# Optimization experiments

Hardware: AMD Instinct MI355X
Metric: run time of the kernel (lower is better)

## Reference

```python
import jax, jax.numpy as jnp
import numpy as np

N_CLASSES = 4
ALPHA = 2.0
BIG = jnp.float32(1e9)  # stands in for +inf at non-site pixels


def _dt1d_sq(f):
    # Exact 1D squared distance transform along the last axis:
    # out[i] = min_j f[j] + (i - j)^2  (brute-force lower envelope, fully vectorized)
    n = f.shape[-1]
    i = jnp.arange(n, dtype=f.dtype)
    d2 = (i[:, None] - i[None, :]) ** 2  # [n, n]
    return jnp.min(f[..., None, :] + d2, axis=-1)


def _edt_sq(sites):
    # Exact squared Euclidean distance to the nearest True pixel (separable 2D DT).
    f = jnp.where(sites, jnp.float32(0.0), BIG)
    f = _dt1d_sq(f)                                  # pass along W
    f = jnp.swapaxes(_dt1d_sq(jnp.swapaxes(f, -1, -2)), -1, -2)  # pass along H
    return f


def _distance_field(img):
    # Mirrors HausdorffDTLoss.distance_field:
    #   fg_dist = edt(fg_mask)  (distance to nearest bg pixel, 0 on bg)
    #   bg_dist = edt(~fg_mask) (distance to nearest fg pixel, 0 on fg)
    #   field = fg_dist + bg_dist if fg_mask.any() else 0
    fg = img > 0.5                                   # [B, H, W] bool
    fg_dist = jnp.sqrt(_edt_sq(~fg))                 # dist to nearest background
    bg_dist = jnp.sqrt(_edt_sq(fg))                  # dist to nearest foreground
    any_fg = jnp.any(fg, axis=(-2, -1), keepdims=True)
    return jnp.where(any_fg, fg_dist + bg_dist, jnp.float32(0.0))


def reference(pred, target):
    # pred: [B, 4, H, W] logits; target: [B, H, W] int labels in [0, 4)
    probs = jax.nn.softmax(pred, axis=1)
    tgt = jnp.moveaxis(jax.nn.one_hot(target, N_CLASSES, dtype=probs.dtype), -1, 1)  # [B,4,H,W]
    total = jnp.float32(0.0)
    for i in range(N_CLASSES):
        p = probs[:, i]
        t = tgt[:, i]
        pred_dt = jax.lax.stop_gradient(_distance_field(p))
        target_dt = jax.lax.stop_gradient(_distance_field(t))
        pred_error = (p - t) ** 2
        distance = pred_dt ** ALPHA + target_dt ** ALPHA
        total = total + jnp.mean(pred_error * distance)
    return total / N_CLASSES


def setup_inputs() -> dict:
    key = jax.random.key(0)
    k1, k2 = jax.random.split(key)
    pred = jax.random.normal(k1, (4, 4, 256, 256), dtype=jnp.float32)
    target = jax.random.randint(k2, (4, 256, 256), 0, 4).astype(jnp.int32)
    return {"pred": pred, "target": target}
```

## Files before the change

### kernel.cpp

```cpp
#include <hip/hip_runtime.h>

#define HH 256
#define WW 256
#define NB 4
#define NC 4
#define NPIX (HH*WW)
#define NIMG (NB*NC)
#define TOTAL (NB*NC*HH*WW)
#define INF_G (1<<30)

__device__ __forceinline__ float wave_reduce(float v) {
    #pragma unroll
    for (int off = 32; off > 0; off >>= 1) v += __shfl_down(v, off);
    return v;
}

__device__ __forceinline__ int nearest_dist(const unsigned long long* m, int x) {
    int best = 0x7fffffff;
    #pragma unroll
    for (int w = 0; w < 4; ++w) {
        unsigned long long mm = m[w];
        if (!mm) continue;
        int rel = x - (w << 6);
        unsigned long long lmask = (rel >= 63) ? ~0ull
                                 : ((rel < 0) ? 0ull : ((2ull << (rel & 63)) - 1ull));
        unsigned long long lm = mm & lmask;
        if (lm) best = min(best, rel - (63 - __clzll(lm)));
        unsigned long long rmask = (rel <= 0) ? ~0ull
                                 : ((rel > 63) ? 0ull : (~0ull << (rel & 63)));
        unsigned long long rm = mm & rmask;
        if (rm) best = min(best, (__ffsll((long long)rm) - 1) - rel);
    }
    return best;
}

__global__ void fused_rows(const float* __restrict__ pred, const int* __restrict__ target,
                           uint2* __restrict__ buf) {
    int blk = blockIdx.x;
    int b = blk >> 8, y = blk & 255;
    int x = threadIdx.x;

    const float* base = pred + (((size_t)b * NC) * HH + y) * WW + x;
    float v0 = base[0 * (size_t)NPIX];
    float v1 = base[1 * (size_t)NPIX];
    float v2 = base[2 * (size_t)NPIX];
    float v3 = base[3 * (size_t)NPIX];
    float m = fmaxf(fmaxf(v0, v1), fmaxf(v2, v3));
    float e0 = expf(v0 - m), e1 = expf(v1 - m), e2 = expf(v2 - m), e3 = expf(v3 - m);
    float inv = 1.0f / (e0 + e1 + e2 + e3);
    float p[4] = { e0 * inv, e1 * inv, e2 * inv, e3 * inv };

    int tc = target[((size_t)b * HH + y) * WW + x];

    __shared__ unsigned long long mP[4][4], mT[4][4];
    int lane = x & 63, wave = x >> 6;
    #pragma unroll
    for (int c = 0; c < 4; ++c) {
        unsigned long long bp = __ballot(p[c] > 0.5f);
        unsigned long long bt = __ballot(tc == c);
        if (lane == 0) { mP[c][wave] = bp; mT[c][wave] = bt; }
    }
    __syncthreads();

    #pragma unroll
    for (int c = 0; c < 4; ++c) {
        bool fgP = p[c] > 0.5f;
        bool fgT = (tc == c);
        unsigned long long flipP = fgP ? ~0ull : 0ull;
        unsigned long long flipT = fgT ? ~0ull : 0ull;
        unsigned long long selP[4], selT[4];
        #pragma unroll
        for (int w = 0; w < 4; ++w) {
            selP[w] = mP[c][w] ^ flipP;
            selT[w] = mT[c][w] ^ flipT;
        }
        int dP = nearest_dist(selP, x);
        int dT = nearest_dist(selT, x);

        unsigned int codeP = (fgP ? 0x100u : 0u) | ((dP > 255) ? 0x200u : (unsigned int)dP);
        unsigned int codeT = (fgT ? 0x100u : 0u) | ((dT > 255) ? 0x200u : (unsigned int)dT);

        float t = fgT ? 1.0f : 0.0f;
        float d = p[c] - t;
        float pe = d * d;

        size_t ti = (((size_t)(b * NC + c)) * WW + x) * HH + y;
        uint2 outv;
        outv.x = codeP | (codeT << 16);
        outv.y = __float_as_uint(pe);
        buf[ti] = outv;
    }
}

__global__ void dt_cols_loss(const uint2* __restrict__ buf, float* __restrict__ partials) {
    int blk = blockIdx.x;
    int img = blk >> 8, x = blk & 255;
    int y = threadIdx.x;
    int lane = y & 63, wv = y >> 6;

    size_t ti = (((size_t)img) * WW + x) * HH + y;

    __shared__ int g[4][HH];
    __shared__ int sF[8];
    __shared__ float sred[4];

    uint2 v = buf[ti];
    unsigned int cP = v.x & 0xFFFFu, cT = v.x >> 16;
    int fgP = (cP >> 8) & 1, emP = (cP >> 9) & 1, dP = (int)(cP & 0xFFu);
    int fgT = (cT >> 8) & 1, emT = (cT >> 9) & 1, dT = (int)(cT & 0xFFu);
    int vP = emP ? INF_G : dP * dP;
    int vT = emT ? INF_G : dT * dT;
    g[0][y] = fgP ? vP : 0;
    g[1][y] = fgP ? 0 : vP;
    g[2][y] = fgT ? vT : 0;
    g[3][y] = fgT ? 0 : vT;

    unsigned long long bP = __ballot(fgP || !emP);
    unsigned long long bT = __ballot(fgT || !emT);
    if (lane == 0) { sF[wv] = (bP != 0ull); sF[4 + wv] = (bT != 0ull); }
    __syncthreads();

    int hs1 = sF[0] | sF[1] | sF[2] | sF[3];
    int hs3 = sF[4] | sF[5] | sF[6] | sF[7];

    const int* gP = fgP ? g[0] : g[1];
    const int* gT = fgT ? g[2] : g[3];

    float dtP, dtT;
    {
        int best = gP[y];
        for (int s = 1; s < HH; ++s) {
            int ss = s * s;
            if (ss >= best) break;
            int jm = y - s;
            if (jm >= 0) best = min(best, gP[jm] + ss);
            int jp = y + s;
            if (jp < HH) best = min(best, gP[jp] + ss);
        }
        dtP = (best >= INF_G) ? sqrtf(1.0e9f) : sqrtf((float)best);
    }
    {
        int best = gT[y];
        for (int s = 1; s < HH; ++s) {
            int ss = s * s;
            if (ss >= best) break;
            int jm = y - s;
            if (jm >= 0) best = min(best, gT[jm] + ss);
            int jp = y + s;
            if (jp < HH) best = min(best, gT[jp] + ss);
        }
        dtT = (best >= INF_G) ? sqrtf(1.0e9f) : sqrtf((float)best);
    }

    float pe = __uint_as_float(v.y);
    float pd = hs1 ? dtP : 0.0f;
    float td = hs3 ? dtT : 0.0f;
    float val = pe * (pd * pd + td * td);

    val = wave_reduce(val);
    if (lane == 0) sred[wv] = val;
    __syncthreads();
    if (y == 0)
        partials[blk] = sred[0] + sred[1] + sred[2] + sred[3];
}

__global__ void final_kernel(const float* __restrict__ partials, float* __restrict__ out) {
    float a = 0.0f;
    for (int i = threadIdx.x; i < 4096; i += 256) a += partials[i];
    a = wave_reduce(a);
    __shared__ float s[4];
    int lane = threadIdx.x & 63, wave = threadIdx.x >> 6;
    if (lane == 0) s[wave] = a;
    __syncthreads();
    if (threadIdx.x == 0)
        out[0] = (s[0] + s[1] + s[2] + s[3]) * (1.0f / (float)TOTAL);
}

extern "C" void kernel_launch(void* const* d_in, const int* in_sizes, int n_in,
                              void* d_out, int out_size, void* d_ws, size_t ws_size,
                              hipStream_t stream) {
    const float* pred  = (const float*)d_in[0];
    const int* target  = (const int*)d_in[1];
    float* out = (float*)d_out;

    float* ws = (float*)d_ws;
    uint2* buf      = (uint2*)ws;
    float* partials = ws + 2097152;

    fused_rows<<<NB * HH, 256, 0, stream>>>(pred, target, buf);
    dt_cols_loss<<<NIMG * WW, 256, 0, stream>>>(buf, partials);
    final_kernel<<<1, 256, 0, stream>>>(partials, out);
}
```

Baseline: 34.41 us.

## Pass compact row bitmasks between kernels and fold final reduction into atomics

The first kernel now writes only per-row ballot bitmasks and a transposed squared-error array, instead of per-pixel packed distance codes. The row-wise nearest-distance search moves into the column kernel, which loads the image's bitmasks into shared memory and handles four columns per 1024-thread block. The separate final reduction kernel is removed: each block atomically adds its scaled partial sum into the output, which the first kernel zeroes. This cuts intermediate global traffic and one launch, at the cost of repeating the row search in the column kernel and a non-deterministic float atomic summation order.

```diff
diff --git a/kernel.cpp b/kernel.cpp
--- a/kernel.cpp
+++ b/kernel.cpp
@@ -34,11 +34,14 @@
     return best;
 }
 
-__global__ void fused_rows(const float* __restrict__ pred, const int* __restrict__ target,
-                           uint2* __restrict__ buf) {
+__global__ void build_masks(const float* __restrict__ pred, const int* __restrict__ target,
+                            unsigned long long* __restrict__ masks, float* __restrict__ peT,
+                            float* __restrict__ out) {
     int blk = blockIdx.x;
     int b = blk >> 8, y = blk & 255;
     int x = threadIdx.x;
+
+    if (blk == 0 && x == 0) out[0] = 0.0f;
 
     const float* base = pred + (((size_t)b * NC) * HH + y) * WW + x;
     float v0 = base[0 * (size_t)NPIX];
@@ -52,79 +55,82 @@
 
     int tc = target[((size_t)b * HH + y) * WW + x];
 
-    __shared__ unsigned long long mP[4][4], mT[4][4];
-    int lane = x & 63, wave = x >> 6;
+    __shared__ unsigned long long sm[NC][2][4];
+    int lane = x & 63, wv = x >> 6;
     #pragma unroll
     for (int c = 0; c < 4; ++c) {
         unsigned long long bp = __ballot(p[c] > 0.5f);
         unsigned long long bt = __ballot(tc == c);
-        if (lane == 0) { mP[c][wave] = bp; mT[c][wave] = bt; }
+        if (lane == 0) { sm[c][0][wv] = bp; sm[c][1][wv] = bt; }
+        float t = (tc == c) ? 1.0f : 0.0f;
+        float d = p[c] - t;
+        peT[(((size_t)(b * NC + c)) * WW + x) * HH + y] = d * d;
     }
     __syncthreads();
 
-    #pragma unroll
-    for (int c = 0; c < 4; ++c) {
-        bool fgP = p[c] > 0.5f;
-        bool fgT = (tc == c);
-        unsigned long long flipP = fgP ? ~0ull : 0ull;
-        unsigned long long flipT = fgT ? ~0ull : 0ull;
-        unsigned long long selP[4], selT[4];
-        #pragma unroll
-        for (int w = 0; w < 4; ++w) {
-            selP[w] = mP[c][w] ^ flipP;
-            selT[w] = mT[c][w] ^ flipT;
-        }
-        int dP = nearest_dist(selP, x);
-        int dT = nearest_dist(selT, x);
-
-        unsigned int codeP = (fgP ? 0x100u : 0u) | ((dP > 255) ? 0x200u : (unsigned int)dP);
-        unsigned int codeT = (fgT ? 0x100u : 0u) | ((dT > 255) ? 0x200u : (unsigned int)dT);
-
-        float t = fgT ? 1.0f : 0.0f;
-        float d = p[c] - t;
-        float pe = d * d;
-
-        size_t ti = (((size_t)(b * NC + c)) * WW + x) * HH + y;
-        uint2 outv;
-        outv.x = codeP | (codeT << 16);
-        outv.y = __float_as_uint(pe);
-        buf[ti] = outv;
+    if (x < 32) {
+        int c = x >> 3, s = (x >> 2) & 1, w = x & 3;
+        masks[(((size_t)(b * NC + c) * HH + y) * 2 + s) * 4 + w] = sm[c][s][w];
     }
 }
 
-__global__ void dt_cols_loss(const uint2* __restrict__ buf, float* __restrict__ partials) {
-    int blk = blockIdx.x;
-    int img = blk >> 8, x = blk & 255;
-    int y = threadIdx.x;
-    int lane = y & 63, wv = y >> 6;
+__global__ __launch_bounds__(1024) void cols_loss(const unsigned long long* __restrict__ masks,
+                                                  const float* __restrict__ peT,
+                                                  float* __restrict__ out) {
+    int bid = blockIdx.x;
+    int img = bid >> 6;
+    int xbase = (bid & 63) << 2;
+    int tid = threadIdx.x;
+    int k = tid >> 8, y = tid & 255;
+    int x = xbase + k;
+    int lane = tid & 63, wv = tid >> 6;
 
-    size_t ti = (((size_t)img) * WW + x) * HH + y;
+    __shared__ unsigned long long sm[HH * 8];
+    __shared__ int g[4][4][HH];
+    __shared__ int sF[2][16];
+    __shared__ float sred[16];
 
-    __shared__ int g[4][HH];
-    __shared__ int sF[8];
-    __shared__ float sred[4];
-
-    uint2 v = buf[ti];
-    unsigned int cP = v.x & 0xFFFFu, cT = v.x >> 16;
-    int fgP = (cP >> 8) & 1, emP = (cP >> 9) & 1, dP = (int)(cP & 0xFFu);
-    int fgT = (cT >> 8) & 1, emT = (cT >> 9) & 1, dT = (int)(cT & 0xFFu);
-    int vP = emP ? INF_G : dP * dP;
-    int vT = emT ? INF_G : dT * dT;
-    g[0][y] = fgP ? vP : 0;
-    g[1][y] = fgP ? 0 : vP;
-    g[2][y] = fgT ? vT : 0;
-    g[3][y] = fgT ? 0 : vT;
-
-    unsigned long long bP = __ballot(fgP || !emP);
-    unsigned long long bT = __ballot(fgT || !emT);
-    if (lane == 0) { sF[wv] = (bP != 0ull); sF[4 + wv] = (bT != 0ull); }
+    const unsigned long long* mbase = masks + (size_t)img * HH * 8;
+    sm[tid]        = mbase[tid];
+    sm[tid + 1024] = mbase[tid + 1024];
     __syncthreads();
 
-    int hs1 = sF[0] | sF[1] | sF[2] | sF[3];
-    int hs3 = sF[4] | sF[5] | sF[6] | sF[7];
+    unsigned long long mp[4], mt[4];
+    #pragma unroll
+    for (int w = 0; w < 4; ++w) { mp[w] = sm[y * 8 + w]; mt[w] = sm[y * 8 + 4 + w]; }
 
-    const int* gP = fgP ? g[0] : g[1];
-    const int* gT = fgT ? g[2] : g[3];
+    int fgP = (int)((mp[x >> 6] >> (x & 63)) & 1);
+    int fgT = (int)((mt[x >> 6] >> (x & 63)) & 1);
+
+    unsigned long long sel[4];
+    unsigned long long flipP = fgP ? ~0ull : 0ull;
+    #pragma unroll
+    for (int w = 0; w < 4; ++w) sel[w] = mp[w] ^ flipP;
+    int dP = nearest_dist(sel, x);
+    int vP = (dP > 255) ? INF_G : dP * dP;
+
+    unsigned long long flipT = fgT ? ~0ull : 0ull;
+    #pragma unroll
+    for (int w = 0; w < 4; ++w) sel[w] = mt[w] ^ flipT;
+    int dT = nearest_dist(sel, x);
+    int vT = (dT > 255) ? INF_G : dT * dT;
+
+    g[k][0][y] = fgP ? vP : 0;
+    g[k][1][y] = fgP ? 0 : vP;
+    g[k][2][y] = fgT ? vT : 0;
+    g[k][3][y] = fgT ? 0 : vT;
+
+    unsigned long long bP = __ballot((mp[0] | mp[1] | mp[2] | mp[3]) != 0ull);
+    unsigned long long bT = __ballot((mt[0] | mt[1] | mt[2] | mt[3]) != 0ull);
+    if (lane == 0) { sF[0][wv] = (bP != 0ull); sF[1][wv] = (bT != 0ull); }
+    __syncthreads();
+
+    int hs1 = 0, hs3 = 0;
+    #pragma unroll
+    for (int i = 0; i < 16; ++i) { hs1 |= sF[0][i]; hs3 |= sF[1][i]; }
+
+    const int* gP = fgP ? g[k][0] : g[k][1];
+    const int* gT = fgT ? g[k][2] : g[k][3];
 
     float dtP, dtT;
     {
@@ -152,7 +158,7 @@
         dtT = (best >= INF_G) ? sqrtf(1.0e9f) : sqrtf((float)best);
     }
 
-    float pe = __uint_as_float(v.y);
+    float pe = peT[((size_t)img * WW + x) * HH + y];
     float pd = hs1 ? dtP : 0.0f;
     float td = hs3 ? dtT : 0.0f;
     float val = pe * (pd * pd + td * td);
@@ -160,20 +166,12 @@
     val = wave_reduce(val);
     if (lane == 0) sred[wv] = val;
     __syncthreads();
-    if (y == 0)
-        partials[blk] = sred[0] + sred[1] + sred[2] + sred[3];
-}
-
-__global__ void final_kernel(const float* __restrict__ partials, float* __restrict__ out) {
-    float a = 0.0f;
-    for (int i = threadIdx.x; i < 4096; i += 256) a += partials[i];
-    a = wave_reduce(a);
-    __shared__ float s[4];
-    int lane = threadIdx.x & 63, wave = threadIdx.x >> 6;
-    if (lane == 0) s[wave] = a;
-    __syncthreads();
-    if (threadIdx.x == 0)
-        out[0] = (s[0] + s[1] + s[2] + s[3]) * (1.0f / (float)TOTAL);
+    if (tid == 0) {
+        float blocksum = 0.0f;
+        #pragma unroll
+        for (int i = 0; i < 16; ++i) blocksum += sred[i];
+        unsafeAtomicAdd(out, blocksum * (1.0f / (float)TOTAL));
+    }
 }
 
 extern "C" void kernel_launch(void* const* d_in, const int* in_sizes, int n_in,
@@ -184,10 +182,9 @@
     float* out = (float*)d_out;
 
     float* ws = (float*)d_ws;
-    uint2* buf      = (uint2*)ws;
-    float* partials = ws + 2097152;
+    unsigned long long* masks = (unsigned long long*)ws;
+    float* peT = ws + 65536;
 
-    fused_rows<<<NB * HH, 256, 0, stream>>>(pred, target, buf);
-    dt_cols_loss<<<NIMG * WW, 256, 0, stream>>>(buf, partials);
-    final_kernel<<<1, 256, 0, stream>>>(partials, out);
+    build_masks<<<NB * HH, 256, 0, stream>>>(pred, target, masks, peT, out);
+    cols_loss<<<NIMG * 64, 1024, 0, stream>>>(masks, peT, out);
 }
```

Result: slower. 36.98 us (+7.5%).
